# Kernel tuning notes

Hardware: AMD Instinct MI355X
Metric: run time of the kernel (lower is better)

## Reference

```python
import jax, jax.numpy as jnp
import numpy as np

B, C, H, DK = 4, 5, 200, 20   # batch, cdd_length, his_length, projected dim
D_INNER = 400                 # Linear(400,1) fan-in


def setup_inputs() -> dict:
    key = jax.random.key(0)
    ks = jax.random.split(key, 8)
    Q = jax.random.normal(ks[0], (B, C, H, D_INNER, DK), jnp.float32)
    K = jax.random.normal(ks[1], (B, C, H, D_INNER, DK), jnp.float32)
    V = jax.random.normal(ks[2], (B, C, H, D_INNER, DK), jnp.float32)
    cdd = jax.random.normal(ks[3], (B, C, H, DK, DK), jnp.float32)
    # nn.Linear(400,1) weight/bias (weight stored as a vector of fan-in size)
    W = jax.random.normal(ks[4], (D_INNER,), jnp.float32) / np.sqrt(D_INNER)
    b = jax.random.normal(ks[5], (), jnp.float32) * 0.01
    # nn.Linear(20,1)
    W1 = jax.random.normal(ks[6], (DK,), jnp.float32) / np.sqrt(DK)
    b1 = jax.random.normal(ks[7], (), jnp.float32) * 0.01
    return {"Q": Q, "K": K, "V": V, "cdd": cdd, "W": W, "b": b, "W1": W1, "b1": b1, "d_k": DK}


def reference(Q, K, V, cdd, W, b, W1, b1, d_k):
    Bs, Cs, Hs = Q.shape[:3]

    def proj(x, w, bb):
        # x.view(B,C,H,-1,20).transpose(-1,-2) -> [B,C,H,20,n]; Linear(n,1).squeeze(-1) -> [B,C,H,20]
        x = x.reshape(Bs, Cs, Hs, -1, 20)       # [B,C,H,n,20]
        x = jnp.swapaxes(x, -1, -2)             # [B,C,H,20,n]
        return jnp.einsum('bchdn,n->bchd', x, w) + bb

    q = proj(Q, W, b)      # [B,C,H,20]
    k = proj(K, W, b)
    v = proj(V, W, b)
    c = proj(cdd, W1, b1)  # [B,C,H,20]

    inv_sqrt_dk = 1.0 / jnp.sqrt(jnp.float32(d_k))
    # scores1 = Q K^T, scores2 = K cdd^T over the his_length axis -> [B,C,H,H]
    scores = (jnp.einsum('bchd,bcgd->bchg', q, k)
              + jnp.einsum('bchd,bcgd->bchg', k, c)) * inv_sqrt_dk
    s = jnp.exp(scores)                                    # no max-subtraction, as in source
    attn = s / (jnp.sum(s, axis=-1, keepdims=True) + 1e-8)
    context = jnp.einsum('bchg,bcgd->bchd', attn, v)       # [B,C,H,20]
    return context, attn
```

## Files before the change

### kernel.cpp

```cpp
#include <hip/hip_runtime.h>

#define BB 4
#define CC 5
#define HH 200
#define DKk 20
#define DI 400
#define NPOS (BB*CC*HH)
#define SEGS 4
#define NSEG (DI/SEGS)

__global__ __launch_bounds__(256, 1) void proj_kernel(
    const float* __restrict__ Q,
    const float* __restrict__ K,
    const float* __restrict__ V,
    const float* __restrict__ cdd,
    const float* __restrict__ W,
    const float* __restrict__ bptr,
    const float* __restrict__ W1,
    const float* __restrict__ b1ptr,
    float* __restrict__ proj)
{
    __shared__ float sW[DI];
    __shared__ float sW1[DKk];
    for (int i = threadIdx.x; i < DI; i += 256) sW[i] = W[i];
    if (threadIdx.x < DKk) sW1[threadIdx.x] = W1[threadIdx.x];
    __syncthreads();

    int tg     = blockIdx.x * 256 + threadIdx.x;
    int seg    = tg & 3;
    int pq     = tg >> 2;
    int quad   = pq % 5;
    int pg     = pq / 5;
    int tensor = pg / NPOS;
    int pos    = pg % NPOS;

    float a0 = 0.f, a1 = 0.f, a2 = 0.f, a3 = 0.f;

    if (tensor < 3) {
        const float* base = (tensor == 0) ? Q : (tensor == 1) ? K : V;
        const float* src  = base + (size_t)pos * (DI * DKk) + quad * 4;
        const int n0 = seg * NSEG;

        for (int ii = 0; ii < 96; ii += 16) {
            float4 x[16];
            #pragma unroll
            for (int j = 0; j < 16; ++j)
                x[j] = *reinterpret_cast<const float4*>(src + (size_t)(n0 + ii + j) * DKk);
            #pragma unroll
            for (int j = 0; j < 16; ++j) {
                float wn = sW[n0 + ii + j];
                a0 += wn * x[j].x;
                a1 += wn * x[j].y;
                a2 += wn * x[j].z;
                a3 += wn * x[j].w;
            }
        }
        {
            float4 x[4];
            #pragma unroll
            for (int j = 0; j < 4; ++j)
                x[j] = *reinterpret_cast<const float4*>(src + (size_t)(n0 + 96 + j) * DKk);
            #pragma unroll
            for (int j = 0; j < 4; ++j) {
                float wn = sW[n0 + 96 + j];
                a0 += wn * x[j].x;
                a1 += wn * x[j].y;
                a2 += wn * x[j].z;
                a3 += wn * x[j].w;
            }
        }
    } else {
        const float* src = cdd + (size_t)pos * (DKk * DKk) + quad * 4;
        const int n0 = seg * 5;
        float4 x[5];
        #pragma unroll
        for (int j = 0; j < 5; ++j)
            x[j] = *reinterpret_cast<const float4*>(src + (size_t)(n0 + j) * DKk);
        #pragma unroll
        for (int j = 0; j < 5; ++j) {
            float wn = sW1[n0 + j];
            a0 += wn * x[j].x;
            a1 += wn * x[j].y;
            a2 += wn * x[j].z;
            a3 += wn * x[j].w;
        }
    }

    a0 += __shfl_xor(a0, 1); a0 += __shfl_xor(a0, 2);
    a1 += __shfl_xor(a1, 1); a1 += __shfl_xor(a1, 2);
    a2 += __shfl_xor(a2, 1); a2 += __shfl_xor(a2, 2);
    a3 += __shfl_xor(a3, 1); a3 += __shfl_xor(a3, 2);

    if (seg == 0) {
        float bias = (tensor < 3) ? bptr[0] : b1ptr[0];
        float4 o; o.x = a0 + bias; o.y = a1 + bias; o.z = a2 + bias; o.w = a3 + bias;
        *reinterpret_cast<float4*>(proj + ((size_t)tensor * NPOS + pos) * DKk + quad * 4) = o;
    }
}

__global__ __launch_bounds__(256) void attn_kernel(
    const float* __restrict__ proj,
    float* __restrict__ attn_out,
    float* __restrict__ ctx_out)
{
    __shared__ float sk[HH * DKk];
    __shared__ float sc[HH * DKk];
    __shared__ float sv[HH * DKk];

    int bc   = blockIdx.x / 25;
    int tile = blockIdx.x % 25;
    int t    = threadIdx.x;

    const float* kp = proj + ((size_t)1 * NPOS + bc * HH) * DKk;
    const float* vp = proj + ((size_t)2 * NPOS + bc * HH) * DKk;
    const float* cp = proj + ((size_t)3 * NPOS + bc * HH) * DKk;

    for (int i = t; i < HH * DKk / 4; i += 256) {
        reinterpret_cast<float4*>(sk)[i] = reinterpret_cast<const float4*>(kp)[i];
        reinterpret_cast<float4*>(sc)[i] = reinterpret_cast<const float4*>(cp)[i];
        reinterpret_cast<float4*>(sv)[i] = reinterpret_cast<const float4*>(vp)[i];
    }
    __syncthreads();

    int row = t >> 5;
    int sub = t & 31;
    int h   = tile * 8 + row;
    int rowIdx = bc * HH + h;

    const float* qr_p = proj + ((size_t)0 * NPOS + rowIdx) * DKk;
    const float* kr_p = proj + ((size_t)1 * NPOS + rowIdx) * DKk;
    float qr[DKk], kr[DKk];
    #pragma unroll
    for (int i = 0; i < 5; ++i) {
        float4 a = reinterpret_cast<const float4*>(qr_p)[i];
        qr[4*i] = a.x; qr[4*i+1] = a.y; qr[4*i+2] = a.z; qr[4*i+3] = a.w;
        float4 b = reinterpret_cast<const float4*>(kr_p)[i];
        kr[4*i] = b.x; kr[4*i+1] = b.y; kr[4*i+2] = b.z; kr[4*i+3] = b.w;
    }

    const float inv_sqrt = 0.22360679774997896f;
    float ctx[DKk];
    #pragma unroll
    for (int d = 0; d < DKk; ++d) ctx[d] = 0.f;
    float rs = 0.f;
    float sreg[7];

    #pragma unroll
    for (int kk = 0; kk < 7; ++kk) {
        int g = sub + 32 * kk;
        float s = 0.f;
        if (g < HH) {
            float dot = 0.f;
            #pragma unroll
            for (int i = 0; i < 5; ++i) {
                float4 kg = reinterpret_cast<const float4*>(sk + g * DKk)[i];
                float4 cg = reinterpret_cast<const float4*>(sc + g * DKk)[i];
                dot += qr[4*i]   * kg.x + qr[4*i+1] * kg.y
                     + qr[4*i+2] * kg.z + qr[4*i+3] * kg.w;
                dot += kr[4*i]   * cg.x + kr[4*i+1] * cg.y
                     + kr[4*i+2] * cg.z + kr[4*i+3] * cg.w;
            }
            s = __expf(dot * inv_sqrt);
            #pragma unroll
            for (int i = 0; i < 5; ++i) {
                float4 vg = reinterpret_cast<const float4*>(sv + g * DKk)[i];
                ctx[4*i]   += s * vg.x;
                ctx[4*i+1] += s * vg.y;
                ctx[4*i+2] += s * vg.z;
                ctx[4*i+3] += s * vg.w;
            }
        }
        sreg[kk] = s;
        rs += s;
    }

    #pragma unroll
    for (int off = 16; off >= 1; off >>= 1)
        rs += __shfl_xor(rs, off, 32);
    float inv = 1.0f / (rs + 1e-8f);

    #pragma unroll
    for (int off = 16; off >= 1; off >>= 1) {
        #pragma unroll
        for (int d = 0; d < DKk; ++d)
            ctx[d] += __shfl_down(ctx[d], (unsigned)off, 32);
    }

    if (sub == 0) {
        float* co = ctx_out + (size_t)rowIdx * DKk;
        #pragma unroll
        for (int i = 0; i < 5; ++i) {
            float4 o;
            o.x = ctx[4*i]   * inv;
            o.y = ctx[4*i+1] * inv;
            o.z = ctx[4*i+2] * inv;
            o.w = ctx[4*i+3] * inv;
            reinterpret_cast<float4*>(co)[i] = o;
        }
    }

    #pragma unroll
    for (int kk = 0; kk < 7; ++kk) {
        int g = sub + 32 * kk;
        if (g < HH)
            attn_out[(size_t)rowIdx * HH + g] = sreg[kk] * inv;
    }
}

extern "C" void kernel_launch(void* const* d_in, const int* in_sizes, int n_in,
                              void* d_out, int out_size, void* d_ws, size_t ws_size,
                              hipStream_t stream) {
    const float* Q   = (const float*)d_in[0];
    const float* K   = (const float*)d_in[1];
    const float* V   = (const float*)d_in[2];
    const float* cdd = (const float*)d_in[3];
    const float* W   = (const float*)d_in[4];
    const float* b   = (const float*)d_in[5];
    const float* W1  = (const float*)d_in[6];
    const float* b1  = (const float*)d_in[7];

    float* proj = (float*)d_ws;

    float* out      = (float*)d_out;
    float* ctx_out  = out;
    float* attn_out = out + 80000;

    proj_kernel<<<(4 * NPOS * 5 * SEGS) / 256, 256, 0, stream>>>(
        Q, K, V, cdd, W, b, W1, b1, proj);
    attn_kernel<<<CC * BB * 25, 256, 0, stream>>>(proj, attn_out, ctx_out);
}
```

Measured before the change: 371.4 us.

## Assign one wavefront per projected position with full-row loads and wave reduction

The projection kernel now maps one 64-lane wavefront to each (tensor, position). Each lane reads whole 80-byte rows of the 400x20 slab, so the wave reads contiguous memory and accumulates all 20 outputs in registers. Weights are read straight from global memory instead of LDS, and a 6-step butterfly shuffle reduces the 20 accumulators across the wave. This targets coalescing and DRAM bandwidth in the memory-bound projection, at the cost of many shuffles per position and idle lanes on the small cdd slabs.

```diff
diff --git a/kernel.cpp b/kernel.cpp
--- a/kernel.cpp
+++ b/kernel.cpp
@@ -6,8 +6,6 @@
 #define DKk 20
 #define DI 400
 #define NPOS (BB*CC*HH)
-#define SEGS 4
-#define NSEG (DI/SEGS)
 
 __global__ __launch_bounds__(256, 1) void proj_kernel(
     const float* __restrict__ Q,
@@ -20,81 +18,99 @@
     const float* __restrict__ b1ptr,
     float* __restrict__ proj)
 {
-    __shared__ float sW[DI];
-    __shared__ float sW1[DKk];
-    for (int i = threadIdx.x; i < DI; i += 256) sW[i] = W[i];
-    if (threadIdx.x < DKk) sW1[threadIdx.x] = W1[threadIdx.x];
-    __syncthreads();
-
-    int tg     = blockIdx.x * 256 + threadIdx.x;
-    int seg    = tg & 3;
-    int pq     = tg >> 2;
-    int quad   = pq % 5;
-    int pg     = pq / 5;
-    int tensor = pg / NPOS;
-    int pos    = pg % NPOS;
-
-    float a0 = 0.f, a1 = 0.f, a2 = 0.f, a3 = 0.f;
+    const int wave = threadIdx.x >> 6;
+    const int lane = threadIdx.x & 63;
+    const int wid  = blockIdx.x * 4 + wave;
+    const int tensor = wid / NPOS;
+    const int pos    = wid % NPOS;
+
+    float acc[DKk];
+    #pragma unroll
+    for (int d = 0; d < DKk; ++d) acc[d] = 0.f;
 
     if (tensor < 3) {
         const float* base = (tensor == 0) ? Q : (tensor == 1) ? K : V;
-        const float* src  = base + (size_t)pos * (DI * DKk) + quad * 4;
-        const int n0 = seg * NSEG;
-
-        for (int ii = 0; ii < 96; ii += 16) {
-            float4 x[16];
-            #pragma unroll
-            for (int j = 0; j < 16; ++j)
-                x[j] = *reinterpret_cast<const float4*>(src + (size_t)(n0 + ii + j) * DKk);
-            #pragma unroll
-            for (int j = 0; j < 16; ++j) {
-                float wn = sW[n0 + ii + j];
-                a0 += wn * x[j].x;
-                a1 += wn * x[j].y;
-                a2 += wn * x[j].z;
-                a3 += wn * x[j].w;
-            }
-        }
-        {
-            float4 x[4];
-            #pragma unroll
-            for (int j = 0; j < 4; ++j)
-                x[j] = *reinterpret_cast<const float4*>(src + (size_t)(n0 + 96 + j) * DKk);
-            #pragma unroll
-            for (int j = 0; j < 4; ++j) {
-                float wn = sW[n0 + 96 + j];
-                a0 += wn * x[j].x;
-                a1 += wn * x[j].y;
-                a2 += wn * x[j].z;
-                a3 += wn * x[j].w;
+        const float4* src = reinterpret_cast<const float4*>(
+            base + (size_t)pos * (DI * DKk));
+
+        float w[6];
+        #pragma unroll
+        for (int i = 0; i < 6; ++i) w[i] = W[lane + 64 * i];
+
+        #pragma unroll
+        for (int half = 0; half < 2; ++half) {
+            float4 x[3][5];
+            #pragma unroll
+            for (int r = 0; r < 3; ++r) {
+                const int n = lane + 64 * (half * 3 + r);
+                #pragma unroll
+                for (int q = 0; q < 5; ++q)
+                    x[r][q] = src[n * 5 + q];
+            }
+            #pragma unroll
+            for (int r = 0; r < 3; ++r) {
+                const float wn = w[half * 3 + r];
+                #pragma unroll
+                for (int q = 0; q < 5; ++q) {
+                    acc[4*q+0] += wn * x[r][q].x;
+                    acc[4*q+1] += wn * x[r][q].y;
+                    acc[4*q+2] += wn * x[r][q].z;
+                    acc[4*q+3] += wn * x[r][q].w;
+                }
+            }
+        }
+        if (lane < DI - 6 * 64) {
+            const int n = lane + 6 * 64;
+            const float wn = W[n];
+            float4 x[5];
+            #pragma unroll
+            for (int q = 0; q < 5; ++q) x[q] = src[n * 5 + q];
+            #pragma unroll
+            for (int q = 0; q < 5; ++q) {
+                acc[4*q+0] += wn * x[q].x;
+                acc[4*q+1] += wn * x[q].y;
+                acc[4*q+2] += wn * x[q].z;
+                acc[4*q+3] += wn * x[q].w;
             }
         }
     } else {
-        const float* src = cdd + (size_t)pos * (DKk * DKk) + quad * 4;
-        const int n0 = seg * 5;
-        float4 x[5];
-        #pragma unroll
-        for (int j = 0; j < 5; ++j)
-            x[j] = *reinterpret_cast<const float4*>(src + (size_t)(n0 + j) * DKk);
-        #pragma unroll
-        for (int j = 0; j < 5; ++j) {
-            float wn = sW1[n0 + j];
-            a0 += wn * x[j].x;
-            a1 += wn * x[j].y;
-            a2 += wn * x[j].z;
-            a3 += wn * x[j].w;
-        }
-    }
-
-    a0 += __shfl_xor(a0, 1); a0 += __shfl_xor(a0, 2);
-    a1 += __shfl_xor(a1, 1); a1 += __shfl_xor(a1, 2);
-    a2 += __shfl_xor(a2, 1); a2 += __shfl_xor(a2, 2);
-    a3 += __shfl_xor(a3, 1); a3 += __shfl_xor(a3, 2);
-
-    if (seg == 0) {
-        float bias = (tensor < 3) ? bptr[0] : b1ptr[0];
-        float4 o; o.x = a0 + bias; o.y = a1 + bias; o.z = a2 + bias; o.w = a3 + bias;
-        *reinterpret_cast<float4*>(proj + ((size_t)tensor * NPOS + pos) * DKk + quad * 4) = o;
+        const float4* src = reinterpret_cast<const float4*>(
+            cdd + (size_t)pos * (DKk * DKk));
+        if (lane < DKk) {
+            const float wn = W1[lane];
+            float4 x[5];
+            #pragma unroll
+            for (int q = 0; q < 5; ++q) x[q] = src[lane * 5 + q];
+            #pragma unroll
+            for (int q = 0; q < 5; ++q) {
+                acc[4*q+0] += wn * x[q].x;
+                acc[4*q+1] += wn * x[q].y;
+                acc[4*q+2] += wn * x[q].z;
+                acc[4*q+3] += wn * x[q].w;
+            }
+        }
+    }
+
+    #pragma unroll
+    for (int m = 32; m >= 1; m >>= 1) {
+        #pragma unroll
+        for (int d = 0; d < DKk; ++d)
+            acc[d] += __shfl_xor(acc[d], m);
+    }
+
+    if (lane == 0) {
+        const float bias = (tensor < 3) ? bptr[0] : b1ptr[0];
+        float4* dst = reinterpret_cast<float4*>(
+            proj + ((size_t)tensor * NPOS + pos) * DKk);
+        #pragma unroll
+        for (int q = 0; q < 5; ++q) {
+            float4 o;
+            o.x = acc[4*q+0] + bias;
+            o.y = acc[4*q+1] + bias;
+            o.z = acc[4*q+2] + bias;
+            o.w = acc[4*q+3] + bias;
+            dst[q] = o;
+        }
     }
 }
 
@@ -225,7 +241,7 @@
     float* ctx_out  = out;
     float* attn_out = out + 80000;
 
-    proj_kernel<<<(4 * NPOS * 5 * SEGS) / 256, 256, 0, stream>>>(
+    proj_kernel<<<4000, 256, 0, stream>>>(
         Q, K, V, cdd, W, b, W1, b1, proj);
     attn_kernel<<<CC * BB * 25, 256, 0, stream>>>(proj, attn_out, ctx_out);
 }
```

After: 487.1 us. 31.2% more time.
